# Kernel tuning notes

Hardware: AMD Instinct MI355X
Metric: run time of the kernel (lower is better)

## Reference

```python
import jax, jax.numpy as jnp
import numpy as np

N_NODES = 100000
N_EDGES = 3200000
IN_DIM, HID_DIM, OUT_DIM = 512, 256, 64


def setup_inputs() -> dict:
    key = jax.random.key(0)
    k1, k2, k3, k4, k5, k6 = jax.random.split(key, 6)
    x = jax.random.normal(k1, (N_NODES, IN_DIM), dtype=jnp.float32)
    src = jax.random.randint(k2, (N_EDGES,), 0, N_NODES, dtype=jnp.int32)
    dst = jax.random.randint(k3, (N_EDGES,), 0, N_NODES, dtype=jnp.int32)
    edge_index = jnp.stack([src, dst])  # [2, E]: row 0 = src (column), row 1 = dst (row)
    edge_weight = jax.random.uniform(k4, (N_EDGES,), dtype=jnp.float32)
    # Xavier-uniform init like nn.init.xavier_uniform_
    lim1 = float(np.sqrt(6.0 / (IN_DIM + HID_DIM)))
    lim2 = float(np.sqrt(6.0 / (HID_DIM + OUT_DIM)))
    W1 = jax.random.uniform(k5, (IN_DIM, HID_DIM), minval=-lim1, maxval=lim1, dtype=jnp.float32)
    W2 = jax.random.uniform(k6, (HID_DIM, OUT_DIM), minval=-lim2, maxval=lim2, dtype=jnp.float32)
    return {"x": x, "edge_index": edge_index, "edge_weight": edge_weight, "W1": W1, "W2": W2}


def _spmm(edge_index, edge_weight, support):
    # out[dst] += w * support[src]  (sparse adjacency @ dense support)
    src, dst = edge_index[0], edge_index[1]
    msgs = support[src] * edge_weight[:, None]  # [E, F]
    return jax.ops.segment_sum(msgs, dst, num_segments=N_NODES)


def reference(x, edge_index, edge_weight, W1, W2):
    # Layer 1: dense GEMM then SpMM, then ReLU (dropout is identity in eval)
    h = _spmm(edge_index, edge_weight, x @ W1)
    h = jax.nn.relu(h)
    # Layer 2
    out = _spmm(edge_index, edge_weight, h @ W2)
    return jax.nn.softmax(out, axis=1)
```

## Files before the change

kernel.cpp:

```cpp
#include <hip/hip_runtime.h>
#include <hip/hip_bf16.h>

typedef __attribute__((ext_vector_type(8))) short bf16x8;
typedef __attribute__((ext_vector_type(4))) float f32x4;
typedef __attribute__((ext_vector_type(4))) _Float16 f16x4;
typedef unsigned short ushort_t;

#define NN   100000
#define NE   3200000
#define IND  512
#define HIDD 256
#define OUTD 64

#define NBKT 98
#define P1E  2048

__device__ __forceinline__ ushort_t f2bf(float a) {
    unsigned u = __float_as_uint(a);
    unsigned r = (u + 0x7FFFu + ((u >> 16) & 1u)) >> 16;
    return (ushort_t)r;
}
__device__ __forceinline__ float bf2f(ushort_t b) {
    return __uint_as_float(((unsigned)b) << 16);
}

union U8 { ushort_t us[8]; unsigned u32[4]; uint4 v; };

#define GLOAD_LDS16(gp, lp) \
    __builtin_amdgcn_global_load_lds( \
        (const __attribute__((address_space(1))) void*)(const void*)(gp), \
        (__attribute__((address_space(3))) void*)(void*)(lp), 16, 0, 0)

__device__ __forceinline__ void split8(float4 v0, float4 v1, bf16x8& aH, bf16x8& aL) {
    float vv[8] = {v0.x, v0.y, v0.z, v0.w, v1.x, v1.y, v1.z, v1.w};
    U8 H, L;
    #pragma unroll
    for (int j = 0; j < 4; ++j) {
        unsigned u0 = __float_as_uint(vv[2 * j]);
        unsigned u1 = __float_as_uint(vv[2 * j + 1]);
        H.u32[j] = __builtin_amdgcn_perm(u1, u0, 0x07060302u);
        float r0 = vv[2 * j]     - __uint_as_float(u0 & 0xFFFF0000u);
        float r1 = vv[2 * j + 1] - __uint_as_float(u1 & 0xFFFF0000u);
        L.u32[j] = __builtin_amdgcn_perm(__float_as_uint(r1),
                                         __float_as_uint(r0), 0x07060302u);
    }
    aH = *(const bf16x8*)&H.v;
    aL = *(const bf16x8*)&L.v;
}

__global__ void splitw_k(const float* __restrict__ in, ushort_t* __restrict__ thi,
                         ushort_t* __restrict__ tlo, int R, int C) {
    int i = blockIdx.x * 256 + threadIdx.x;
    if (i < R * C) {
        int r = i / C, c = i % C;
        float a = in[i];
        ushort_t h = f2bf(a);
        thi[(size_t)c * R + r] = h;
        tlo[(size_t)c * R + r] = f2bf(a - bf2f(h));
    }
}

__global__ __launch_bounds__(256, 3) void gemm1_k(
    const float* __restrict__ A, const ushort_t* __restrict__ BtHi,
    const ushort_t* __restrict__ BtLo, _Float16* __restrict__ C)
{
    const int M = NN, N = HIDD, K = IND;
    __shared__ __align__(16) float    sA [128 * 32];
    __shared__ __align__(16) ushort_t sBh[128 * 32];
    __shared__ __align__(16) ushort_t sBl[128 * 32];

    const int tid  = threadIdx.x;
    const int wave = tid >> 6;
    const int lane = tid & 63;
    const int quad = lane >> 4;
    const int l15  = lane & 15;
    const int wr   = wave >> 1;
    const int wc   = wave & 1;
    const int n0   = blockIdx.x * 128;
    const int m0   = blockIdx.y * 128;

    const float* aSrc[4];
    float*       aDst[4];
    #pragma unroll
    for (int it = 0; it < 4; ++it) {
        int f = it * 256 + tid;
        int r = f >> 3;
        int bp = (f & 7) ^ ((r & 3) << 1) ^ ((r >> 2) & 1);
        int gr = m0 + r; if (gr >= M) gr = M - 1;
        aSrc[it] = A + (size_t)gr * K + bp * 4;
        aDst[it] = &sA[f * 4];
    }
    const ushort_t* bhSrc[2]; const ushort_t* blSrc[2];
    ushort_t* bhDst[2]; ushort_t* blDst[2];
    #pragma unroll
    for (int it = 0; it < 2; ++it) {
        int f = it * 256 + tid;
        int r = f >> 2;
        int qp = (f & 3) ^ ((r >> 1) & 3);
        bhSrc[it] = BtHi + (size_t)(n0 + r) * K + qp * 8;
        blSrc[it] = BtLo + (size_t)(n0 + r) * K + qp * 8;
        bhDst[it] = &sBh[f * 8];
        blDst[it] = &sBl[f * 8];
    }

    int aOff[4][2];
    #pragma unroll
    for (int ms = 0; ms < 4; ++ms) {
        int rA = wr * 64 + ms * 16 + l15;
        int sw = ((rA & 3) << 1) ^ ((rA >> 2) & 1);
        int cb = quad << 1;
        aOff[ms][0] = rA * 32 + (((cb    ) ^ sw) << 2);
        aOff[ms][1] = rA * 32 + (((cb | 1) ^ sw) << 2);
    }
    int bOff[4];
    #pragma unroll
    for (int ns = 0; ns < 4; ++ns) {
        int rB = wc * 64 + ns * 16 + l15;
        bOff[ns] = rB * 32 + (quad ^ ((rB >> 1) & 3)) * 8;
    }

    f32x4 acc[4][4] = {};

    for (int k0 = 0; k0 < K; k0 += 32) {
        #pragma unroll
        for (int it = 0; it < 4; ++it) GLOAD_LDS16(aSrc[it] + k0, aDst[it]);
        #pragma unroll
        for (int it = 0; it < 2; ++it) {
            GLOAD_LDS16(bhSrc[it] + k0, bhDst[it]);
            GLOAD_LDS16(blSrc[it] + k0, blDst[it]);
        }
        __syncthreads();

        bf16x8 aH[4], aL[4];
        #pragma unroll
        for (int ms = 0; ms < 4; ++ms) {
            float4 v0 = *(const float4*)&sA[aOff[ms][0]];
            float4 v1 = *(const float4*)&sA[aOff[ms][1]];
            split8(v0, v1, aH[ms], aL[ms]);
        }

        #pragma unroll
        for (int ns = 0; ns < 4; ++ns) {
            bf16x8 bH = *(const bf16x8*)&sBh[bOff[ns]];
            bf16x8 bL = *(const bf16x8*)&sBl[bOff[ns]];
            #pragma unroll
            for (int ms = 0; ms < 4; ++ms) {
                acc[ms][ns] = __builtin_amdgcn_mfma_f32_16x16x32_bf16(aH[ms], bH, acc[ms][ns], 0, 0, 0);
                acc[ms][ns] = __builtin_amdgcn_mfma_f32_16x16x32_bf16(aL[ms], bH, acc[ms][ns], 0, 0, 0);
                acc[ms][ns] = __builtin_amdgcn_mfma_f32_16x16x32_bf16(aH[ms], bL, acc[ms][ns], 0, 0, 0);
            }
        }
        __syncthreads();
    }

    #pragma unroll
    for (int ms = 0; ms < 4; ++ms) {
        int row = m0 + wr * 64 + ms * 16 + quad * 4;
        #pragma unroll
        for (int ns = 0; ns < 4; ++ns) {
            int col = n0 + wc * 64 + ns * 16 + l15;
            #pragma unroll
            for (int r = 0; r < 4; ++r)
                if (row + r < M) C[(size_t)(row + r) * N + col] = (_Float16)acc[ms][ns][r];
        }
    }
}

__global__ __launch_bounds__(256) void bhist_k(const int* __restrict__ dst,
                                               int* __restrict__ bucketHist) {
    __shared__ int h[NBKT];
    int t = threadIdx.x;
    if (t < NBKT) h[t] = 0;
    __syncthreads();
    #pragma unroll
    for (int j = 0; j < 4; ++j) {
        int e = blockIdx.x * 1024 + t + j * 256;
        if (e < NE) atomicAdd(&h[dst[e] >> 10], 1);
    }
    __syncthreads();
    if (t < NBKT && h[t]) atomicAdd(&bucketHist[t], h[t]);
}

__global__ __launch_bounds__(128) void bscan_k(const int* __restrict__ bucketHist,
                                               int* __restrict__ bucketStart,
                                               int* __restrict__ bucketCursor) {
    __shared__ int s[128];
    int t = threadIdx.x;
    int v = (t < NBKT) ? bucketHist[t] : 0;
    s[t] = v;
    for (int off = 1; off < 128; off <<= 1) {
        __syncthreads();
        int a = (t >= off) ? s[t - off] : 0;
        __syncthreads();
        s[t] += a;
    }
    __syncthreads();
    if (t < NBKT) { bucketStart[t] = s[t] - v; bucketCursor[t] = s[t] - v; }
    if (t == NBKT - 1) bucketStart[NBKT] = s[t];
}

__global__ __launch_bounds__(256) void phase1_k(
    const int* __restrict__ src, const int* __restrict__ dst,
    const float* __restrict__ w, int* __restrict__ bucketCursor,
    int2* __restrict__ binned)
{
    __shared__ int2 raw[P1E];
    __shared__ int2 ord[P1E];
    __shared__ ushort_t rbkt[P1E], obkt[P1E];
    __shared__ int hist[128], excl[128], cursor[128], gbase[128], stmp[128];

    int t = threadIdx.x;
    if (t < 128) hist[t] = 0;
    __syncthreads();

    int e0 = blockIdx.x * P1E;
    #pragma unroll
    for (int j = 0; j < P1E / 256; ++j) {
        int li = t + j * 256;
        int e = e0 + li;
        if (e < NE) {
            int d = dst[e];
            int b = d >> 10;
            raw[li] = make_int2(src[e] | ((d & 1023) << 17), __float_as_int(w[e]));
            rbkt[li] = (ushort_t)b;
            atomicAdd(&hist[b], 1);
        } else rbkt[li] = 0xFFFFu;
    }
    __syncthreads();
    int v = (t < 128) ? hist[t] : 0;
    if (t < 128) stmp[t] = v;
    for (int off = 1; off < 128; off <<= 1) {
        __syncthreads();
        int a = (t < 128 && t >= off) ? stmp[t - off] : 0;
        __syncthreads();
        if (t < 128) stmp[t] += a;
    }
    __syncthreads();
    if (t < 128) { excl[t] = stmp[t] - v; cursor[t] = stmp[t] - v; }
    if (t < NBKT) gbase[t] = atomicAdd(&bucketCursor[t], hist[t]);
    __syncthreads();
    #pragma unroll
    for (int j = 0; j < P1E / 256; ++j) {
        int li = t + j * 256;
        ushort_t b = rbkt[li];
        if (b != 0xFFFFu) {
            int p = atomicAdd(&cursor[b], 1);
            ord[p] = raw[li];
            obkt[p] = b;
        }
    }
    __syncthreads();
    int tot = excl[NBKT - 1] + hist[NBKT - 1];
    #pragma unroll
    for (int j = 0; j < P1E / 256; ++j) {
        int li = t + j * 256;
        if (li < tot) {
            int b = obkt[li];
            binned[(size_t)gbase[b] + (li - excl[b])] = ord[li];
        }
    }
}

__global__ __launch_bounds__(256) void phase2_k(
    const int* __restrict__ bucketStart, const int2* __restrict__ binned,
    int* __restrict__ rowptr, int2* __restrict__ esw)
{
    __shared__ int cnt[1024], ex[1024], cur[1024], wsum[256];
    int t = threadIdx.x, blk = blockIdx.x;
    int gb = bucketStart[blk], ge = bucketStart[blk + 1];
    #pragma unroll
    for (int j = 0; j < 4; ++j) cnt[t + j * 256] = 0;
    __syncthreads();
    for (int e = gb + t; e < ge; e += 256)
        atomicAdd(&cnt[(binned[e].x >> 17) & 1023], 1);
    __syncthreads();
    int b4 = t * 4;
    int l0 = cnt[b4], l1 = cnt[b4 + 1], l2 = cnt[b4 + 2], l3 = cnt[b4 + 3];
    int ls = l0 + l1 + l2 + l3;
    wsum[t] = ls;
    for (int off = 1; off < 256; off <<= 1) {
        __syncthreads();
        int a = (t >= off) ? wsum[t - off] : 0;
        __syncthreads();
        wsum[t] += a;
    }
    __syncthreads();
    int be = wsum[t] - ls;
    ex[b4] = be;            cur[b4] = be;
    ex[b4 + 1] = be + l0;     cur[b4 + 1] = be + l0;
    ex[b4 + 2] = be + l0 + l1;  cur[b4 + 2] = be + l0 + l1;
    ex[b4 + 3] = be + l0 + l1 + l2; cur[b4 + 3] = be + l0 + l1 + l2;
    __syncthreads();
    int n0 = blk << 10;
    #pragma unroll
    for (int j = 0; j < 4; ++j) {
        int i = b4 + j;
        if (n0 + i < NN) rowptr[n0 + i] = gb + ex[i];
    }
    if (blk == NBKT - 1 && t == 0) rowptr[NN] = NE;
    for (int e = gb + t; e < ge; e += 256) {
        int2 en = binned[e];
        int d = (en.x >> 17) & 1023;
        int p = atomicAdd(&cur[d], 1);
        esw[(size_t)gb + p] = make_int2(en.x & 0x1FFFF, en.y);
    }
}

__global__ __launch_bounds__(256) void spmm_relu_gemm2_k(
    const int* __restrict__ rowptr, const int2* __restrict__ esw,
    const _Float16* __restrict__ X, const ushort_t* __restrict__ BtHi,
    const ushort_t* __restrict__ BtLo, _Float16* __restrict__ S2)
{
    __shared__ __align__(16) float h[16][260];

    const int wave  = threadIdx.x >> 6;
    const int lane  = threadIdx.x & 63;
    const int quad  = lane >> 4;
    const int l15   = lane & 15;
    const int nbase = blockIdx.x * 16;

    const _Float16* Xl = X + lane * 4;
    #pragma unroll
    for (int i = 0; i < 4; ++i) {
        const int ln   = wave * 4 + i;
        const int node = nbase + ln;
        const int beg = rowptr[node], end = rowptr[node + 1];
        f32x4 acc = {0.f, 0.f, 0.f, 0.f};
        #pragma unroll 8
        for (int e = beg; e < end; ++e) {
            int2 sw = esw[e];
            float w = __int_as_float(sw.y);
            f16x4 v = *(const f16x4*)(Xl + (size_t)sw.x * HIDD);
            acc.x += (float)v[0] * w;
            acc.y += (float)v[1] * w;
            acc.z += (float)v[2] * w;
            acc.w += (float)v[3] * w;
        }
        f32x4 r;
        r.x = fmaxf(acc.x, 0.f);
        r.y = fmaxf(acc.y, 0.f);
        r.z = fmaxf(acc.z, 0.f);
        r.w = fmaxf(acc.w, 0.f);
        *(f32x4*)&h[ln][lane * 4] = r;
    }
    __syncthreads();

    f32x4 acc2 = {0.f, 0.f, 0.f, 0.f};
    const ushort_t* bh = BtHi + (size_t)(wave * 16 + l15) * HIDD;
    const ushort_t* bl = BtLo + (size_t)(wave * 16 + l15) * HIDD;
    #pragma unroll
    for (int ks = 0; ks < 8; ++ks) {
        const int ko = ks * 32 + quad * 8;
        const float* ap = &h[l15][ko];
        float4 v0 = *(const float4*)ap;
        float4 v1 = *(const float4*)(ap + 4);
        bf16x8 aH, aL;
        split8(v0, v1, aH, aL);
        bf16x8 bH = *(const bf16x8*)(bh + ko);
        bf16x8 bL = *(const bf16x8*)(bl + ko);
        acc2 = __builtin_amdgcn_mfma_f32_16x16x32_bf16(aH, bH, acc2, 0, 0, 0);
        acc2 = __builtin_amdgcn_mfma_f32_16x16x32_bf16(aL, bH, acc2, 0, 0, 0);
        acc2 = __builtin_amdgcn_mfma_f32_16x16x32_bf16(aH, bL, acc2, 0, 0, 0);
    }
    #pragma unroll
    for (int r = 0; r < 4; ++r) {
        const int node = nbase + quad * 4 + r;
        S2[(size_t)node * OUTD + wave * 16 + l15] = (_Float16)acc2[r];
    }
}

__global__ __launch_bounds__(256) void spmm_softmax_k(
    const int* __restrict__ rowptr, const int2* __restrict__ esw,
    const _Float16* __restrict__ X, float* __restrict__ out)
{
    int node = blockIdx.x * 4 + (threadIdx.x >> 6);
    int lane = threadIdx.x & 63;
    int beg = rowptr[node], end = rowptr[node + 1];
    float acc = 0.f;
    #pragma unroll 4
    for (int e = beg; e < end; ++e) {
        int2 sw = esw[e];
        acc += __int_as_float(sw.y) * (float)X[(size_t)sw.x * OUTD + lane];
    }
    float mx = acc;
    #pragma unroll
    for (int off = 32; off > 0; off >>= 1) mx = fmaxf(mx, __shfl_xor(mx, off));
    float ex = __expf(acc - mx);
    float sm = ex;
    #pragma unroll
    for (int off = 32; off > 0; off >>= 1) sm += __shfl_xor(sm, off);
    out[(size_t)node * OUTD + lane] = ex / sm;
}

extern "C" void kernel_launch(void* const* d_in, const int* in_sizes, int n_in,
                              void* d_out, int out_size, void* d_ws, size_t ws_size,
                              hipStream_t stream) {
    const float* x  = (const float*)d_in[0];
    const int*   ei = (const int*)d_in[1];
    const float* ew = (const float*)d_in[2];
    const float* W1 = (const float*)d_in[3];
    const float* W2 = (const float*)d_in[4];
    float* out = (float*)d_out;
    const int* src = ei;
    const int* dst = ei + NE;

    char* ws = (char*)d_ws;
    size_t o = 0;
    auto take = [&](size_t bytes) -> void* {
        void* p = (void*)(ws + o);
        o += (bytes + 255) & ~(size_t)255;
        return p;
    };
    _Float16* S1      = (_Float16*)take((size_t)NN * HIDD * 2);
    _Float16* S2      = (_Float16*)take((size_t)NN * OUTD * 2);
    int2*     binned  = (int2*    )take((size_t)NE * 8);
    ushort_t* W1tHi   = (ushort_t*)take((size_t)IND * HIDD * 2);
    ushort_t* W1tLo   = (ushort_t*)take((size_t)IND * HIDD * 2);
    ushort_t* W2tHi   = (ushort_t*)take((size_t)HIDD * OUTD * 2);
    ushort_t* W2tLo   = (ushort_t*)take((size_t)HIDD * OUTD * 2);
    int*      rowptr  = (int*     )take((size_t)(NN + 1) * 4);
    int*      bHist   = (int*     )take(NBKT * 4);
    int*      bStart  = (int*     )take((NBKT + 1) * 4);
    int*      bCursor = (int*     )take(NBKT * 4);
    int2*     esw     = (int2*    )take((size_t)NE * 8);
    (void)in_sizes; (void)n_in; (void)out_size; (void)ws_size;

    const int MB = (NN + 127) / 128;

    hipMemsetAsync(bHist, 0, NBKT * 4, stream);
    splitw_k<<<(IND * HIDD + 255) / 256, 256, 0, stream>>>(W1, W1tHi, W1tLo, IND, HIDD);
    splitw_k<<<(HIDD * OUTD + 255) / 256, 256, 0, stream>>>(W2, W2tHi, W2tLo, HIDD, OUTD);

    bhist_k<<<(NE + 1023) / 1024, 256, 0, stream>>>(dst, bHist);
    bscan_k<<<1, 128, 0, stream>>>(bHist, bStart, bCursor);
    phase1_k<<<(NE + P1E - 1) / P1E, 256, 0, stream>>>(src, dst, ew, bCursor, binned);
    phase2_k<<<NBKT, 256, 0, stream>>>(bStart, binned, rowptr, esw);

    gemm1_k<<<dim3(2, MB), 256, 0, stream>>>(x, W1tHi, W1tLo, S1);
    spmm_relu_gemm2_k<<<NN / 16, 256, 0, stream>>>(rowptr, esw, S1, W2tHi, W2tLo, S2);
    spmm_softmax_k<<<NN / 4, 256, 0, stream>>>(rowptr, esw, S2, out);
}
```

Baseline: 898.8 us.

## Sort nodes by degree for load-balanced fused SpMM+GEMM2 blocks

```diff
diff --git a/kernel.cpp b/kernel.cpp
--- a/kernel.cpp
+++ b/kernel.cpp
@@ -14,6 +14,7 @@
 
 #define NBKT 98
 #define P1E  2048
+#define DBIN 512
 
 __device__ __forceinline__ ushort_t f2bf(float a) {
     unsigned u = __float_as_uint(a);
@@ -306,24 +307,68 @@
     }
 }
 
+__global__ __launch_bounds__(256) void dhist_k(const int* __restrict__ rowptr,
+                                               int* __restrict__ dhist) {
+    int i = blockIdx.x * 256 + threadIdx.x;
+    if (i < NN) {
+        int d = rowptr[i + 1] - rowptr[i];
+        int key = (DBIN - 1) - min(d, DBIN - 1);
+        atomicAdd(&dhist[key], 1);
+    }
+}
+
+__global__ __launch_bounds__(DBIN) void dscan_k(const int* __restrict__ dhist,
+                                                int* __restrict__ dcur) {
+    __shared__ int s[DBIN];
+    int t = threadIdx.x;
+    int v = dhist[t];
+    s[t] = v;
+    for (int off = 1; off < DBIN; off <<= 1) {
+        __syncthreads();
+        int a = (t >= off) ? s[t - off] : 0;
+        __syncthreads();
+        s[t] += a;
+    }
+    __syncthreads();
+    dcur[t] = s[t] - v;
+}
+
+__global__ __launch_bounds__(256) void dscatter_k(const int* __restrict__ rowptr,
+                                                  int* __restrict__ dcur,
+                                                  int* __restrict__ perm) {
+    int i = blockIdx.x * 256 + threadIdx.x;
+    if (i < NN) {
+        int d = rowptr[i + 1] - rowptr[i];
+        int key = (DBIN - 1) - min(d, DBIN - 1);
+        int p = atomicAdd(&dcur[key], 1);
+        perm[p] = i;
+    }
+}
+
 __global__ __launch_bounds__(256) void spmm_relu_gemm2_k(
-    const int* __restrict__ rowptr, const int2* __restrict__ esw,
-    const _Float16* __restrict__ X, const ushort_t* __restrict__ BtHi,
-    const ushort_t* __restrict__ BtLo, _Float16* __restrict__ S2)
+    const int* __restrict__ perm, const int* __restrict__ rowptr,
+    const int2* __restrict__ esw, const _Float16* __restrict__ X,
+    const ushort_t* __restrict__ BtHi, const ushort_t* __restrict__ BtLo,
+    _Float16* __restrict__ S2)
 {
     __shared__ __align__(16) float h[16][260];
-
-    const int wave  = threadIdx.x >> 6;
-    const int lane  = threadIdx.x & 63;
+    __shared__ int nodes[16];
+
+    const int tid   = threadIdx.x;
+    const int wave  = tid >> 6;
+    const int lane  = tid & 63;
     const int quad  = lane >> 4;
     const int l15   = lane & 15;
     const int nbase = blockIdx.x * 16;
 
+    if (tid < 16) nodes[tid] = perm[nbase + tid];
+    __syncthreads();
+
     const _Float16* Xl = X + lane * 4;
     #pragma unroll
     for (int i = 0; i < 4; ++i) {
         const int ln   = wave * 4 + i;
-        const int node = nbase + ln;
+        const int node = nodes[ln];
         const int beg = rowptr[node], end = rowptr[node + 1];
         f32x4 acc = {0.f, 0.f, 0.f, 0.f};
         #pragma unroll 8
@@ -364,7 +409,7 @@
     }
     #pragma unroll
     for (int r = 0; r < 4; ++r) {
-        const int node = nbase + quad * 4 + r;
+        const int node = nodes[quad * 4 + r];
         S2[(size_t)node * OUTD + wave * 16 + l15] = (_Float16)acc2[r];
     }
 }
@@ -423,11 +468,15 @@
     int*      bStart  = (int*     )take((NBKT + 1) * 4);
     int*      bCursor = (int*     )take(NBKT * 4);
     int2*     esw     = (int2*    )take((size_t)NE * 8);
+    int*      dhist   = (int*     )take(DBIN * 4);
+    int*      dcur    = (int*     )take(DBIN * 4);
+    int*      perm    = (int*     )take((size_t)NN * 4);
     (void)in_sizes; (void)n_in; (void)out_size; (void)ws_size;
 
     const int MB = (NN + 127) / 128;
 
     hipMemsetAsync(bHist, 0, NBKT * 4, stream);
+    hipMemsetAsync(dhist, 0, DBIN * 4, stream);
     splitw_k<<<(IND * HIDD + 255) / 256, 256, 0, stream>>>(W1, W1tHi, W1tLo, IND, HIDD);
     splitw_k<<<(HIDD * OUTD + 255) / 256, 256, 0, stream>>>(W2, W2tHi, W2tLo, HIDD, OUTD);
 
@@ -436,7 +485,11 @@
     phase1_k<<<(NE + P1E - 1) / P1E, 256, 0, stream>>>(src, dst, ew, bCursor, binned);
     phase2_k<<<NBKT, 256, 0, stream>>>(bStart, binned, rowptr, esw);
 
+    dhist_k<<<(NN + 255) / 256, 256, 0, stream>>>(rowptr, dhist);
+    dscan_k<<<1, DBIN, 0, stream>>>(dhist, dcur);
+    dscatter_k<<<(NN + 255) / 256, 256, 0, stream>>>(rowptr, dcur, perm);
+
     gemm1_k<<<dim3(2, MB), 256, 0, stream>>>(x, W1tHi, W1tLo, S1);
-    spmm_relu_gemm2_k<<<NN / 16, 256, 0, stream>>>(rowptr, esw, S1, W2tHi, W2tLo, S2);
+    spmm_relu_gemm2_k<<<NN / 16, 256, 0, stream>>>(perm, rowptr, esw, S1, W2tHi, W2tLo, S2);
     spmm_softmax_k<<<NN / 4, 256, 0, stream>>>(rowptr, esw, S2, out);
 }
```

After: 1.258 ms. 1.4x slower.
